# Performance work log

Hardware: AMD Instinct MI355X
Metric: run time of the kernel (lower is better)

The kernel has to match this reference:

```python
import jax, jax.numpy as jnp
import numpy as np

N = 500_000
E = 16_000_000
G = 5_000
F_IN = 64
DIM = 10


def _mlp(x, W1, b1, W2, b2):
    return jnp.maximum(x @ W1 + b1, 0.0) @ W2 + b2


def setup_inputs() -> dict:
    key = jax.random.key(0)
    ks = jax.random.split(key, 32)
    inp = {
        "h": jax.random.normal(ks[0], (N, F_IN), dtype=jnp.float32),
        "src": jax.random.randint(ks[1], (E,), 0, N, dtype=jnp.int32),
        "dst": jax.random.randint(ks[2], (E,), 0, N, dtype=jnp.int32),
        "node_graph": jnp.sort(jax.random.randint(ks[3], (N,), 0, G, dtype=jnp.int32)),
    }
    k = 4
    for i in range(1, 6):
        d_in = F_IN if i == 1 else DIM
        inp[f"W1_{i}"] = jax.random.normal(ks[k], (d_in, DIM), dtype=jnp.float32) * 0.1; k += 1
        inp[f"b1_{i}"] = jnp.zeros((DIM,), dtype=jnp.float32)
        inp[f"W2_{i}"] = jax.random.normal(ks[k], (DIM, DIM), dtype=jnp.float32) * 0.1; k += 1
        inp[f"b2_{i}"] = jnp.zeros((DIM,), dtype=jnp.float32)
        inp[f"l_{i}"] = jax.random.normal(ks[k], (DIM, 1), dtype=jnp.float32) * 0.1; k += 1
    return inp


def reference(h, src, dst, node_graph,
              W1_1, b1_1, W2_1, b2_1, l_1,
              W1_2, b1_2, W2_2, b2_2, l_2,
              W1_3, b1_3, W2_3, b2_3, l_3,
              W1_4, b1_4, W2_4, b2_4, l_4,
              W1_5, b1_5, W2_5, b2_5, l_5):
    # GINConv with eps=0: out = MLP(h + sum_{j in N(i)} h_j), then outer ReLU
    def gin(x, W1, b1, W2, b2):
        agg = jax.ops.segment_sum(x[src], dst, num_segments=N)
        return jnp.maximum(_mlp(x + agg, W1, b1, W2, b2), 0.0)

    x1 = gin(h, W1_1, b1_1, W2_1, b2_1)
    x2 = gin(x1, W1_2, b1_2, W2_2, b2_2)
    x3 = gin(x2, W1_3, b1_3, W2_3, b2_3)
    x4 = gin(x3, W1_4, b1_4, W2_4, b2_4)
    x5 = gin(x4, W1_5, b1_5, W2_5, b2_5)

    counts = jax.ops.segment_sum(jnp.ones((N,), dtype=jnp.float32), node_graph, num_segments=G)
    counts = jnp.maximum(counts, 1.0)[:, None]  # [G,1]

    def mean_nodes(x):
        return jax.ops.segment_sum(x, node_graph, num_segments=G) / counts

    s = (mean_nodes(x1) @ l_1 + mean_nodes(x2) @ l_2 + mean_nodes(x3) @ l_3
         + mean_nodes(x4) @ l_4 + mean_nodes(x5) @ l_5)  # [G,1]
    return jax.nn.sigmoid(s)
```

## Files before the change

### kernel.cpp

```cpp
#include <hip/hip_runtime.h>


#define SENTINEL 0xFFFFFFFFu

__device__ __forceinline__ unsigned short f2bf(float f) {
    unsigned b = __float_as_uint(f);
    b += 0x7fffu + ((b >> 16) & 1u);
    return (unsigned short)(b >> 16);
}
__device__ __forceinline__ float bflo(unsigned u) { return __uint_as_float(u << 16); }
__device__ __forceinline__ float bfhi(unsigned u) { return __uint_as_float(u & 0xffff0000u); }

__global__ void k1_hw1_bf16(const float* __restrict__ h, const float* __restrict__ W1,
                            unsigned* __restrict__ y, int N) {
    __shared__ float sW[640];
    for (int i = threadIdx.x; i < 640; i += blockDim.x) sW[i] = W1[i];
    __syncthreads();
    int n = blockIdx.x * blockDim.x + threadIdx.x;
    if (n >= N) return;
    const float* hr = h + (size_t)n * 64;
    float acc[10];
#pragma unroll
    for (int j = 0; j < 10; j++) acc[j] = 0.f;
#pragma unroll 4
    for (int k = 0; k < 64; k += 4) {
        float4 hv = *(const float4*)(hr + k);
#pragma unroll
        for (int j = 0; j < 10; j++) {
            acc[j] += hv.x * sW[(k + 0) * 10 + j];
            acc[j] += hv.y * sW[(k + 1) * 10 + j];
            acc[j] += hv.z * sW[(k + 2) * 10 + j];
            acc[j] += hv.w * sW[(k + 3) * 10 + j];
        }
    }
    unsigned r0 = (unsigned)f2bf(acc[0]) | ((unsigned)f2bf(acc[1]) << 16);
    unsigned r1 = (unsigned)f2bf(acc[2]) | ((unsigned)f2bf(acc[3]) << 16);
    unsigned r2 = (unsigned)f2bf(acc[4]) | ((unsigned)f2bf(acc[5]) << 16);
    unsigned r3 = (unsigned)f2bf(acc[6]) | ((unsigned)f2bf(acc[7]) << 16);
    unsigned r4 = (unsigned)f2bf(acc[8]) | ((unsigned)f2bf(acc[9]) << 16);
    unsigned* yr = y + (size_t)n * 8;
    *(uint4*)yr = make_uint4(r0, r1, r2, r3);
    yr[4] = r4;
}

__global__ void k1_hw1_f32(const float* __restrict__ h, const float* __restrict__ W1,
                           float* __restrict__ y, int N) {
    __shared__ float sW[640];
    for (int i = threadIdx.x; i < 640; i += blockDim.x) sW[i] = W1[i];
    __syncthreads();
    int n = blockIdx.x * blockDim.x + threadIdx.x;
    if (n >= N) return;
    const float* hr = h + (size_t)n * 64;
    float acc[10];
#pragma unroll
    for (int j = 0; j < 10; j++) acc[j] = 0.f;
#pragma unroll 4
    for (int k = 0; k < 64; k += 4) {
        float4 hv = *(const float4*)(hr + k);
#pragma unroll
        for (int j = 0; j < 10; j++) {
            acc[j] += hv.x * sW[(k + 0) * 10 + j];
            acc[j] += hv.y * sW[(k + 1) * 10 + j];
            acc[j] += hv.z * sW[(k + 2) * 10 + j];
            acc[j] += hv.w * sW[(k + 3) * 10 + j];
        }
    }
    float* yr = y + (size_t)n * 16;
#pragma unroll
    for (int j = 0; j < 10; j++) yr[j] = acc[j];
}

__global__ void k_bhist(const int* __restrict__ dst, unsigned* __restrict__ bucket_cnt,
                        int E) {
    __shared__ unsigned h[512];
    int t = threadIdx.x;
    h[t] = 0; h[t + 256] = 0;
    __syncthreads();
    int stride = gridDim.x * blockDim.x;
    for (int e = blockIdx.x * blockDim.x + t; e < E; e += stride)
        atomicAdd(&h[(unsigned)dst[e] >> 10], 1u);
    __syncthreads();
    if (h[t]) atomicAdd(&bucket_cnt[t], h[t]);
    if (h[t + 256]) atomicAdd(&bucket_cnt[t + 256], h[t + 256]);
}

__global__ void k_bscan(const unsigned* __restrict__ bucket_cnt,
                        unsigned* __restrict__ bbase, unsigned* __restrict__ bcur, int B) {
    __shared__ unsigned s[512];
    int t = threadIdx.x;
    unsigned v = (t < B) ? bucket_cnt[t] : 0u;
    s[t] = v;
    __syncthreads();
    for (int off = 1; off < 512; off <<= 1) {
        unsigned u = (t >= off) ? s[t - off] : 0u;
        __syncthreads();
        s[t] += u;
        __syncthreads();
    }
    unsigned excl = s[t] - v;
    if (t < B) { bbase[t] = excl; bcur[t] = excl; }
    if (t == B - 1) bbase[B] = s[t];
}

__global__ __launch_bounds__(1024) void k_bscatter2(
        const int* __restrict__ src, const int* __restrict__ dst,
        unsigned* __restrict__ bcur, unsigned* __restrict__ pairs,
        int E, int nblocks) {
    __shared__ unsigned cnt[512];
    int t = threadIdx.x;
    int per = (E + nblocks - 1) / nblocks;
    int beg = blockIdx.x * per;
    int end = beg + per; if (end > E) end = E;
    if (beg >= E) return;
    if (t < 512) cnt[t] = 0;
    __syncthreads();
    for (int e = beg + t; e < end; e += 1024)
        atomicAdd(&cnt[(unsigned)dst[e] >> 10], 1u);
    __syncthreads();
    unsigned c = 0, base = 0;
    if (t < 512) { c = cnt[t]; if (c) base = atomicAdd(&bcur[t], c); }
    __syncthreads();
    if (t < 512) cnt[t] = base;
    __syncthreads();
    for (int e = beg + t; e < end; e += 1024) {
        unsigned d = (unsigned)dst[e];
        unsigned pos = atomicAdd(&cnt[d >> 10], 1u);
        pairs[pos] = ((unsigned)src[e] << 10) | (d & 1023u);
    }
}

__global__ __launch_bounds__(1024) void k_p2(
        const unsigned* __restrict__ pairs, const unsigned* __restrict__ bbase,
        unsigned* __restrict__ edges, unsigned* __restrict__ row_start,
        int N, int B, int E, int packed) {
    __shared__ unsigned cnt[1024], scn[1024], cur[1024];
    int t = threadIdx.x, b = blockIdx.x;
    unsigned beg = bbase[b], end = bbase[b + 1];
    cnt[t] = 0;
    __syncthreads();
    for (unsigned e = beg + t; e < end; e += 1024)
        atomicAdd(&cnt[pairs[e] & 1023u], 1u);
    __syncthreads();
    unsigned v = cnt[t];
    scn[t] = v;
    __syncthreads();
    for (int off = 1; off < 1024; off <<= 1) {
        unsigned u = (t >= off) ? scn[t - off] : 0u;
        __syncthreads();
        scn[t] += u;
        __syncthreads();
    }
    unsigned excl = scn[t] - v;
    int node = (b << 10) + t;
    if (node < N) row_start[node] = beg + excl;
    if (b == B - 1 && t == 0) row_start[N] = (unsigned)E;
    cur[t] = beg + excl;
    __syncthreads();
    for (unsigned e = beg + t; e < end; e += 1024) {
        unsigned pv = pairs[e];
        unsigned pos = atomicAdd(&cur[pv & 1023u], 1u);
        edges[pos] = packed ? pv : (pv >> 10);
    }
}

__global__ __launch_bounds__(256) void k_layerQ(
        const unsigned* __restrict__ yin, unsigned* __restrict__ yout,
        const unsigned* __restrict__ row_start, const unsigned* __restrict__ edges,
        const float* __restrict__ b1, const float* __restrict__ W2,
        const float* __restrict__ b2, const float* __restrict__ l,
        const float* __restrict__ W1n,
        const int* __restrict__ node_graph, float* __restrict__ gacc,
        int N, int last) {
    __shared__ float sW2[100], sW1[100], sb1[10], sb2[10], sl[10];
    int t = threadIdx.x;
    if (t < 100) sW2[t] = W2[t];
    if (!last && t >= 128 && t < 228) sW1[t - 128] = W1n[t - 128];
    if (t < 10) { sb1[t] = b1[t]; sb2[t] = b2[t]; sl[t] = l[t]; }
    __syncthreads();
    int q = t & 3;
    int n = blockIdx.x * 64 + (t >> 2);
    bool valid = n < N;
    int nc = valid ? n : (N - 1);

    float acc[10];
#pragma unroll
    for (int j = 0; j < 10; j++) acc[j] = 0.f;

    unsigned beg = 0, end = 0;
    if (valid) { beg = row_start[n]; end = row_start[n + 1]; }
    unsigned e = beg + (unsigned)q;
    for (; e + 4 < end; e += 8) {
        unsigned s0 = edges[e];
        unsigned s1 = edges[e + 4];
        const unsigned* p0 = yin + (size_t)s0 * 8;
        const unsigned* p1 = yin + (size_t)s1 * 8;
        uint4 a0 = *(const uint4*)p0;
        unsigned b0 = p0[4];
        uint4 a1 = *(const uint4*)p1;
        unsigned b1v = p1[4];
        acc[0] += bflo(a0.x) + bflo(a1.x);
        acc[1] += bfhi(a0.x) + bfhi(a1.x);
        acc[2] += bflo(a0.y) + bflo(a1.y);
        acc[3] += bfhi(a0.y) + bfhi(a1.y);
        acc[4] += bflo(a0.z) + bflo(a1.z);
        acc[5] += bfhi(a0.z) + bfhi(a1.z);
        acc[6] += bflo(a0.w) + bflo(a1.w);
        acc[7] += bfhi(a0.w) + bfhi(a1.w);
        acc[8] += bflo(b0)   + bflo(b1v);
        acc[9] += bfhi(b0)   + bfhi(b1v);
    }
    if (e < end) {
        unsigned s0 = edges[e];
        const unsigned* p0 = yin + (size_t)s0 * 8;
        uint4 a0 = *(const uint4*)p0;
        unsigned b0 = p0[4];
        acc[0] += bflo(a0.x); acc[1] += bfhi(a0.x);
        acc[2] += bflo(a0.y); acc[3] += bfhi(a0.y);
        acc[4] += bflo(a0.z); acc[5] += bfhi(a0.z);
        acc[6] += bflo(a0.w); acc[7] += bfhi(a0.w);
        acc[8] += bflo(b0);   acc[9] += bfhi(b0);
    }

#pragma unroll
    for (int j = 0; j < 10; j++) acc[j] += __shfl_xor(acc[j], 1);
#pragma unroll
    for (int j = 0; j < 10; j++) acc[j] += __shfl_xor(acc[j], 2);

    const unsigned* yr = yin + (size_t)nc * 8;
    uint4 qa = *(const uint4*)yr;
    unsigned q4 = yr[4];
    acc[0] += bflo(qa.x); acc[1] += bfhi(qa.x);
    acc[2] += bflo(qa.y); acc[3] += bfhi(qa.y);
    acc[4] += bflo(qa.z); acc[5] += bfhi(qa.z);
    acc[6] += bflo(qa.w); acc[7] += bfhi(qa.w);
    acc[8] += bflo(q4);   acc[9] += bfhi(q4);

    float z[10], x[10];
#pragma unroll
    for (int j = 0; j < 10; j++) {
        float v = acc[j] + sb1[j];
        z[j] = v > 0.f ? v : 0.f;
    }
#pragma unroll
    for (int j = 0; j < 10; j++) {
        float v = sb2[j];
#pragma unroll
        for (int k = 0; k < 10; k++) v += z[k] * sW2[k * 10 + j];
        x[j] = v > 0.f ? v : 0.f;
    }
    float p = 0.f;
#pragma unroll
    for (int j = 0; j < 10; j++) p += x[j] * sl[j];
    if (!valid) p = 0.f;
    int g = node_graph[nc];

    int g0 = __shfl(g, 0);
    if (__all(g == g0)) {
#pragma unroll
        for (int off = 32; off > 0; off >>= 1) p += __shfl_down(p, off);
        if ((t & 63) == 0) unsafeAtomicAdd(&gacc[g0], p * 0.25f);
    } else {
        if (valid && q == 0) unsafeAtomicAdd(&gacc[g], p);
    }

    if (!last && valid && q == 0) {
        float yn[10];
#pragma unroll
        for (int j = 0; j < 10; j++) {
            float v = 0.f;
#pragma unroll
            for (int k = 0; k < 10; k++) v += x[k] * sW1[k * 10 + j];
            yn[j] = v;
        }
        unsigned r0 = (unsigned)f2bf(yn[0]) | ((unsigned)f2bf(yn[1]) << 16);
        unsigned r1 = (unsigned)f2bf(yn[2]) | ((unsigned)f2bf(yn[3]) << 16);
        unsigned r2 = (unsigned)f2bf(yn[4]) | ((unsigned)f2bf(yn[5]) << 16);
        unsigned r3 = (unsigned)f2bf(yn[6]) | ((unsigned)f2bf(yn[7]) << 16);
        unsigned r4 = (unsigned)f2bf(yn[8]) | ((unsigned)f2bf(yn[9]) << 16);
        unsigned* yo = yout + (size_t)n * 8;
        *(uint4*)yo = make_uint4(r0, r1, r2, r3);
        yo[4] = r4;
    }
}

__global__ void k4_final(const float* __restrict__ gacc, const int* __restrict__ node_graph,
                         float* __restrict__ out, int N, int G) {
    int g = blockIdx.x * blockDim.x + threadIdx.x;
    if (g >= G) return;
    int lo = 0, hi = N;
    while (lo < hi) { int m = (lo + hi) >> 1; if (node_graph[m] < g) lo = m + 1; else hi = m; }
    int lo2 = lo, hi2 = N;
    while (lo2 < hi2) { int m = (lo2 + hi2) >> 1; if (node_graph[m] <= g) lo2 = m + 1; else hi2 = m; }
    float c = (float)(hi2 - lo);
    if (c < 1.f) c = 1.f;
    float s = gacc[g] / c;
    out[g] = 1.f / (1.f + __expf(-s));
}

__global__ __launch_bounds__(256) void k_layer(
        const float* __restrict__ yin, float* __restrict__ yout,
        const unsigned* __restrict__ row_start, const unsigned* __restrict__ edges,
        const float* __restrict__ b1, const float* __restrict__ W2,
        const float* __restrict__ b2, const float* __restrict__ l,
        const float* __restrict__ W1n,
        const int* __restrict__ node_graph, float* __restrict__ gacc,
        int N, int last) {
    __shared__ float sW2[100], sW1[100], sb1[10], sb2[10], sl[10];
    int t = threadIdx.x;
    if (t < 100) sW2[t] = W2[t];
    if (!last && t >= 128 && t < 228) sW1[t - 128] = W1n[t - 128];
    if (t < 10) { sb1[t] = b1[t]; sb2[t] = b2[t]; sl[t] = l[t]; }
    __syncthreads();
    int n = blockIdx.x * 256 + t;
    bool valid = n < N;
    int nc = valid ? n : (N - 1);
    const float* yr = yin + (size_t)nc * 16;
    float4 a = *(const float4*)yr;
    float4 b = *(const float4*)(yr + 4);
    float2 c = *(const float2*)(yr + 8);
    float acc[10] = {a.x, a.y, a.z, a.w, b.x, b.y, b.z, b.w, c.x, c.y};
    unsigned beg = 0, end = 0;
    if (valid) { beg = row_start[n]; end = row_start[n + 1]; }
    for (unsigned e = beg; e < end; ++e) {
        unsigned s = edges[e];
        const float* pr = yin + (size_t)s * 16;
        float4 pa = *(const float4*)pr;
        float4 pb = *(const float4*)(pr + 4);
        float2 pc = *(const float2*)(pr + 8);
        acc[0] += pa.x; acc[1] += pa.y; acc[2] += pa.z; acc[3] += pa.w;
        acc[4] += pb.x; acc[5] += pb.y; acc[6] += pb.z; acc[7] += pb.w;
        acc[8] += pc.x; acc[9] += pc.y;
    }
    float z[10], x[10];
#pragma unroll
    for (int j = 0; j < 10; j++) {
        float v = acc[j] + sb1[j];
        z[j] = v > 0.f ? v : 0.f;
    }
#pragma unroll
    for (int j = 0; j < 10; j++) {
        float v = sb2[j];
#pragma unroll
        for (int k = 0; k < 10; k++) v += z[k] * sW2[k * 10 + j];
        x[j] = v > 0.f ? v : 0.f;
    }
    float p = 0.f;
#pragma unroll
    for (int j = 0; j < 10; j++) p += x[j] * sl[j];
    if (!valid) p = 0.f;
    int g = node_graph[nc];
    int g0 = __shfl(g, 0);
    if (__all(g == g0)) {
#pragma unroll
        for (int off = 32; off > 0; off >>= 1) p += __shfl_down(p, off);
        if ((t & 63) == 0) unsafeAtomicAdd(&gacc[g0], p);
    } else {
        if (valid) unsafeAtomicAdd(&gacc[g], p);
    }
    if (!last && valid) {
        float yn[10];
#pragma unroll
        for (int j = 0; j < 10; j++) {
            float v = 0.f;
#pragma unroll
            for (int k = 0; k < 10; k++) v += x[k] * sW1[k * 10 + j];
            yn[j] = v;
        }
        float* yo = yout + (size_t)n * 16;
        *(float4*)yo = make_float4(yn[0], yn[1], yn[2], yn[3]);
        *(float4*)(yo + 4) = make_float4(yn[4], yn[5], yn[6], yn[7]);
        *(float2*)(yo + 8) = make_float2(yn[8], yn[9]);
    }
}

static inline size_t al16(size_t w) { return (w + 15) & ~(size_t)15; }

extern "C" void kernel_launch(void* const* d_in, const int* in_sizes, int n_in,
                              void* d_out, int out_size, void* d_ws, size_t ws_size,
                              hipStream_t stream) {
    const float* h  = (const float*)d_in[0];
    const int* src  = (const int*)d_in[1];
    const int* dst  = (const int*)d_in[2];
    const int* ng   = (const int*)d_in[3];
    int N = in_sizes[3];
    int E = in_sizes[1];
    int G = out_size;

    const float* W1[5]; const float* b1[5]; const float* W2[5]; const float* b2[5]; const float* l[5];
    for (int i = 0; i < 5; i++) {
        W1[i] = (const float*)d_in[4 + i * 5 + 0];
        b1[i] = (const float*)d_in[4 + i * 5 + 1];
        W2[i] = (const float*)d_in[4 + i * 5 + 2];
        b2[i] = (const float*)d_in[4 + i * 5 + 3];
        l[i]  = (const float*)d_in[4 + i * 5 + 4];
    }
    float* out = (float*)d_out;

    int B = (N + 1023) >> 10;

    size_t wY   = al16((size_t)N * 8);
    size_t wRg2 = al16(((size_t)E > (size_t)N * 8) ? (size_t)E : (size_t)N * 8);
    size_t wE   = al16((size_t)E);
    size_t wRS  = al16((size_t)N + 1);
    size_t need_r10 = (wY + wRg2 + wE + wRS + 1552 + al16((size_t)G)) * 4;

    size_t regAB = (size_t)N * 16;
    size_t reg2f = ((size_t)E > regAB) ? (size_t)E : regAB;
    size_t need_r4 = (regAB + reg2f + (size_t)E + (size_t)(N + 1) + 1537 + (size_t)G) * 4;

    if (ws_size >= need_r10 && B <= 512) {
        unsigned* y0 = (unsigned*)d_ws;
        unsigned* pairs = y0 + wY;
        unsigned* y1 = pairs;
        unsigned* edges = pairs + wRg2;
        unsigned* row_start = edges + wE;
        unsigned* bucket_cnt = row_start + wRS;
        unsigned* bbase = bucket_cnt + 512;
        unsigned* bcur = bbase + 513;
        float* gacc = (float*)(bcur + 512);

        hipMemsetAsync(bucket_cnt, 0, 512 * 4, stream);
        hipMemsetAsync(gacc, 0, (size_t)G * 4, stream);

        k1_hw1_bf16<<<(N + 255) / 256, 256, 0, stream>>>(h, W1[0], y0, N);

        k_bhist<<<2048, 256, 0, stream>>>(dst, bucket_cnt, E);
        k_bscan<<<1, 512, 0, stream>>>(bucket_cnt, bbase, bcur, B);
        k_bscatter2<<<256, 1024, 0, stream>>>(src, dst, bcur, pairs, E, 256);
        k_p2<<<B, 1024, 0, stream>>>(pairs, bbase, edges, row_start, N, B, E, 0);

        unsigned* ybuf[2] = {y0, y1};
        int qblocks = (N + 63) / 64;
        for (int i = 0; i < 5; i++) {
            k_layerQ<<<qblocks, 256, 0, stream>>>(
                ybuf[i & 1], ybuf[(i + 1) & 1], row_start, edges,
                b1[i], W2[i], b2[i], l[i], i < 4 ? W1[i + 1] : nullptr,
                ng, gacc, N, i == 4 ? 1 : 0);
        }
        k4_final<<<(G + 255) / 256, 256, 0, stream>>>(gacc, ng, out, N, G);
        return;
    }

    if (ws_size >= need_r4 && B <= 512) {
        float* y0 = (float*)d_ws;
        unsigned* pairs = (unsigned*)(y0 + regAB);
        float* y1 = (float*)pairs;
        unsigned* edges = pairs + reg2f;
        unsigned* row_start = edges + E;
        unsigned* bucket_cnt = row_start + (N + 1);
        unsigned* bbase = bucket_cnt + 512;
        unsigned* bcur = bbase + 513;
        float* gacc = (float*)(bcur + 512);

        hipMemsetAsync(bucket_cnt, 0, 512 * 4, stream);
        hipMemsetAsync(gacc, 0, (size_t)G * 4, stream);

        k1_hw1_f32<<<(N + 255) / 256, 256, 0, stream>>>(h, W1[0], y0, N);
        k_bhist<<<2048, 256, 0, stream>>>(dst, bucket_cnt, E);
        k_bscan<<<1, 512, 0, stream>>>(bucket_cnt, bbase, bcur, B);
        k_bscatter2<<<256, 1024, 0, stream>>>(src, dst, bcur, pairs, E, 256);
        k_p2<<<B, 1024, 0, stream>>>(pairs, bbase, edges, row_start, N, B, E, 0);

        float* ybuf[2] = {y0, y1};
        for (int i = 0; i < 5; i++) {
            k_layer<<<(N + 255) / 256, 256, 0, stream>>>(
                ybuf[i & 1], ybuf[(i + 1) & 1], row_start, edges,
                b1[i], W2[i], b2[i], l[i], i < 4 ? W1[i + 1] : nullptr,
                ng, gacc, N, i == 4 ? 1 : 0);
        }
        k4_final<<<(G + 255) / 256, 256, 0, stream>>>(gacc, ng, out, N, G);
    }
}
```

Measured before the change: 1.987 ms.

## Replace atomic bucket-offset scatter with deterministic per-block count/scan radix pass

The first-pass bucketing of edges by destination is restructured. Each of 256 blocks now writes its per-bucket histogram to a grid, a column-wise scan gives each block a fixed base offset per bucket, and the scatter kernel reads those offsets directly. This removes the second read-and-count pass over dst inside the scatter kernel, the global atomics on bucket cursors, and one memset, at the cost of two extra small kernels and a 2x512x256 offset table. The layer kernel also gets a launch-bounds occupancy hint of 8 blocks.

```diff
diff --git a/kernel.cpp b/kernel.cpp
--- a/kernel.cpp
+++ b/kernel.cpp
@@ -1,7 +1,7 @@
 #include <hip/hip_runtime.h>
 
 
-#define SENTINEL 0xFFFFFFFFu
+#define NBLK 256
 
 __device__ __forceinline__ unsigned short f2bf(float f) {
     unsigned b = __float_as_uint(f);
@@ -70,25 +70,45 @@
     for (int j = 0; j < 10; j++) yr[j] = acc[j];
 }
 
-__global__ void k_bhist(const int* __restrict__ dst, unsigned* __restrict__ bucket_cnt,
-                        int E) {
+__global__ __launch_bounds__(1024) void k_cnt(
+        const int* __restrict__ dst, unsigned* __restrict__ gcnt, int E) {
     __shared__ unsigned h[512];
     int t = threadIdx.x;
-    h[t] = 0; h[t + 256] = 0;
-    __syncthreads();
-    int stride = gridDim.x * blockDim.x;
-    for (int e = blockIdx.x * blockDim.x + t; e < E; e += stride)
+    if (t < 512) h[t] = 0;
+    __syncthreads();
+    int per = (E + NBLK - 1) / NBLK;
+    int beg = blockIdx.x * per;
+    int end = beg + per; if (end > E) end = E;
+    for (int e = beg + t; e < end; e += 1024)
         atomicAdd(&h[(unsigned)dst[e] >> 10], 1u);
     __syncthreads();
-    if (h[t]) atomicAdd(&bucket_cnt[t], h[t]);
-    if (h[t + 256]) atomicAdd(&bucket_cnt[t + 256], h[t + 256]);
-}
-
-__global__ void k_bscan(const unsigned* __restrict__ bucket_cnt,
-                        unsigned* __restrict__ bbase, unsigned* __restrict__ bcur, int B) {
+    if (t < 512) gcnt[blockIdx.x * 512 + t] = h[t];
+}
+
+__global__ __launch_bounds__(NBLK) void k_scan2(
+        const unsigned* __restrict__ gcnt, unsigned* __restrict__ gbase,
+        unsigned* __restrict__ btot) {
+    __shared__ unsigned s[NBLK];
+    int b = blockIdx.x;
+    int t = threadIdx.x;
+    unsigned v = gcnt[t * 512 + b];
+    s[t] = v;
+    __syncthreads();
+    for (int off = 1; off < NBLK; off <<= 1) {
+        unsigned u = (t >= off) ? s[t - off] : 0u;
+        __syncthreads();
+        s[t] += u;
+        __syncthreads();
+    }
+    gbase[t * 512 + b] = s[t] - v;
+    if (t == NBLK - 1) btot[b] = s[t];
+}
+
+__global__ void k_bscan(const unsigned* __restrict__ btot,
+                        unsigned* __restrict__ bbase, int B) {
     __shared__ unsigned s[512];
     int t = threadIdx.x;
-    unsigned v = (t < B) ? bucket_cnt[t] : 0u;
+    unsigned v = (t < B) ? btot[t] : 0u;
     s[t] = v;
     __syncthreads();
     for (int off = 1; off < 512; off <<= 1) {
@@ -97,34 +117,24 @@
         s[t] += u;
         __syncthreads();
     }
-    unsigned excl = s[t] - v;
-    if (t < B) { bbase[t] = excl; bcur[t] = excl; }
+    if (t < B) bbase[t] = s[t] - v;
     if (t == B - 1) bbase[B] = s[t];
 }
 
-__global__ __launch_bounds__(1024) void k_bscatter2(
+__global__ __launch_bounds__(1024) void k_scatter(
         const int* __restrict__ src, const int* __restrict__ dst,
-        unsigned* __restrict__ bcur, unsigned* __restrict__ pairs,
-        int E, int nblocks) {
-    __shared__ unsigned cnt[512];
-    int t = threadIdx.x;
-    int per = (E + nblocks - 1) / nblocks;
+        const unsigned* __restrict__ bbase, const unsigned* __restrict__ gbase,
+        unsigned* __restrict__ pairs, int E) {
+    __shared__ unsigned cur[512];
+    int t = threadIdx.x;
+    if (t < 512) cur[t] = bbase[t] + gbase[blockIdx.x * 512 + t];
+    __syncthreads();
+    int per = (E + NBLK - 1) / NBLK;
     int beg = blockIdx.x * per;
     int end = beg + per; if (end > E) end = E;
-    if (beg >= E) return;
-    if (t < 512) cnt[t] = 0;
-    __syncthreads();
-    for (int e = beg + t; e < end; e += 1024)
-        atomicAdd(&cnt[(unsigned)dst[e] >> 10], 1u);
-    __syncthreads();
-    unsigned c = 0, base = 0;
-    if (t < 512) { c = cnt[t]; if (c) base = atomicAdd(&bcur[t], c); }
-    __syncthreads();
-    if (t < 512) cnt[t] = base;
-    __syncthreads();
     for (int e = beg + t; e < end; e += 1024) {
         unsigned d = (unsigned)dst[e];
-        unsigned pos = atomicAdd(&cnt[d >> 10], 1u);
+        unsigned pos = atomicAdd(&cur[d >> 10], 1u);
         pairs[pos] = ((unsigned)src[e] << 10) | (d & 1023u);
     }
 }
@@ -163,7 +173,7 @@
     }
 }
 
-__global__ __launch_bounds__(256) void k_layerQ(
+__global__ __launch_bounds__(256, 8) void k_layerQ(
         const unsigned* __restrict__ yin, unsigned* __restrict__ yout,
         const unsigned* __restrict__ row_start, const unsigned* __restrict__ edges,
         const float* __restrict__ b1, const float* __restrict__ W2,
@@ -402,31 +412,34 @@
     size_t wRg2 = al16(((size_t)E > (size_t)N * 8) ? (size_t)E : (size_t)N * 8);
     size_t wE   = al16((size_t)E);
     size_t wRS  = al16((size_t)N + 1);
-    size_t need_r10 = (wY + wRg2 + wE + wRS + 1552 + al16((size_t)G)) * 4;
+    size_t wGrid = (size_t)NBLK * 512;
+    size_t need_r11 = (wY + wRg2 + wE + wRS + 1040 + 2 * wGrid + al16((size_t)G)) * 4;
 
     size_t regAB = (size_t)N * 16;
     size_t reg2f = ((size_t)E > regAB) ? (size_t)E : regAB;
-    size_t need_r4 = (regAB + reg2f + (size_t)E + (size_t)(N + 1) + 1537 + (size_t)G) * 4;
-
-    if (ws_size >= need_r10 && B <= 512) {
+    size_t need_r4 = (regAB + reg2f + (size_t)E + (size_t)(N + 1) + 1040 +
+                      2 * wGrid + (size_t)G) * 4;
+
+    if (ws_size >= need_r11 && B <= 512) {
         unsigned* y0 = (unsigned*)d_ws;
         unsigned* pairs = y0 + wY;
         unsigned* y1 = pairs;
         unsigned* edges = pairs + wRg2;
         unsigned* row_start = edges + wE;
-        unsigned* bucket_cnt = row_start + wRS;
-        unsigned* bbase = bucket_cnt + 512;
-        unsigned* bcur = bbase + 513;
-        float* gacc = (float*)(bcur + 512);
-
-        hipMemsetAsync(bucket_cnt, 0, 512 * 4, stream);
+        unsigned* btot = row_start + wRS;
+        unsigned* bbase = btot + 512;
+        unsigned* gcnt = bbase + 528;
+        unsigned* gbase = gcnt + wGrid;
+        float* gacc = (float*)(gbase + wGrid);
+
         hipMemsetAsync(gacc, 0, (size_t)G * 4, stream);
 
         k1_hw1_bf16<<<(N + 255) / 256, 256, 0, stream>>>(h, W1[0], y0, N);
 
-        k_bhist<<<2048, 256, 0, stream>>>(dst, bucket_cnt, E);
-        k_bscan<<<1, 512, 0, stream>>>(bucket_cnt, bbase, bcur, B);
-        k_bscatter2<<<256, 1024, 0, stream>>>(src, dst, bcur, pairs, E, 256);
+        k_cnt<<<NBLK, 1024, 0, stream>>>(dst, gcnt, E);
+        k_scan2<<<512, NBLK, 0, stream>>>(gcnt, gbase, btot);
+        k_bscan<<<1, 512, 0, stream>>>(btot, bbase, B);
+        k_scatter<<<NBLK, 1024, 0, stream>>>(src, dst, bbase, gbase, pairs, E);
         k_p2<<<B, 1024, 0, stream>>>(pairs, bbase, edges, row_start, N, B, E, 0);
 
         unsigned* ybuf[2] = {y0, y1};
@@ -447,18 +460,19 @@
         float* y1 = (float*)pairs;
         unsigned* edges = pairs + reg2f;
         unsigned* row_start = edges + E;
-        unsigned* bucket_cnt = row_start + (N + 1);
-        unsigned* bbase = bucket_cnt + 512;
-        unsigned* bcur = bbase + 513;
-        float* gacc = (float*)(bcur + 512);
-
-        hipMemsetAsync(bucket_cnt, 0, 512 * 4, stream);
+        unsigned* btot = row_start + (N + 1);
+        unsigned* bbase = btot + 512;
+        unsigned* gcnt = bbase + 528;
+        unsigned* gbase = gcnt + wGrid;
+        float* gacc = (float*)(gbase + wGrid);
+
         hipMemsetAsync(gacc, 0, (size_t)G * 4, stream);
 
         k1_hw1_f32<<<(N + 255) / 256, 256, 0, stream>>>(h, W1[0], y0, N);
-        k_bhist<<<2048, 256, 0, stream>>>(dst, bucket_cnt, E);
-        k_bscan<<<1, 512, 0, stream>>>(bucket_cnt, bbase, bcur, B);
-        k_bscatter2<<<256, 1024, 0, stream>>>(src, dst, bcur, pairs, E, 256);
+        k_cnt<<<NBLK, 1024, 0, stream>>>(dst, gcnt, E);
+        k_scan2<<<512, NBLK, 0, stream>>>(gcnt, gbase, btot);
+        k_bscan<<<1, 512, 0, stream>>>(btot, bbase, B);
+        k_scatter<<<NBLK, 1024, 0, stream>>>(src, dst, bbase, gbase, pairs, E);
         k_p2<<<B, 1024, 0, stream>>>(pairs, bbase, edges, row_start, N, B, E, 0);
 
         float* ybuf[2] = {y0, y1};
```

Result: slower. 3.316 ms (+66.8%).
